# Performance work log

Hardware: AMD Instinct MI355X
Metric: run time of the kernel (lower is better)

The kernel has to match this reference:

```python
import jax, jax.numpy as jnp
import numpy as np


def _hadamard(n: int) -> np.ndarray:
    # Sylvester construction; n must be a power of 2 (asserted in the torch source).
    H = np.array([[1.0]], dtype=np.float32)
    while H.shape[0] < n:
        H = np.block([[H, H], [H, -H]])
    return (H * (n ** -0.5)).astype(np.float32)


def _rotate_activation(x):
    # hadamard_transform(x, scale=D**-0.5) over the last dim; bf16 in/out like the CUDA kernel.
    D = x.shape[-1]
    H = jnp.asarray(_hadamard(D))
    return (x.astype(jnp.float32) @ H).astype(x.dtype)


def _cu_seqlen_kv_bounds(seq_lens, num_ctx_tokens):
    # Vectorized equivalent of compute_cu_seqlen_kv_bounds_nocache (repeat_interleave -> searchsorted).
    offsets = jnp.concatenate([jnp.zeros(1, jnp.int32), jnp.cumsum(seq_lens).astype(jnp.int32)])
    pos = jnp.arange(num_ctx_tokens, dtype=jnp.int32)
    batch_ids = jnp.searchsorted(offsets, pos, side='right').astype(jnp.int32) - 1
    ks = offsets[batch_ids]                 # start of this token's sequence in packed KV
    ke = ks + (pos - ks) + 1                # causal: local_position + 1 past the start
    return ks, ke


def setup_inputs() -> dict:
    key = jax.random.key(0)
    k1, k2, k3 = jax.random.split(key, 3)
    T, H, D = 2048, 16, 128
    q = jax.random.normal(k1, (T, H, D), dtype=jnp.bfloat16)
    k = jax.random.normal(k2, (T, D), dtype=jnp.bfloat16)
    weights = jax.random.uniform(k3, (T, H), dtype=jnp.float32) * (H ** -0.5)
    seq_lens = jnp.array([1024, 1024], dtype=jnp.int32)
    return {"q": q, "k": k, "weights": weights, "seq_lens": seq_lens, "index_topk": 256}


def reference(q, k, weights, seq_lens, index_topk):
    T = q.shape[0]
    # Hadamard-rotate q and k (lightning indexer activation rotation).
    qr = _rotate_activation(q).astype(jnp.float32)   # [T, H, D]
    kr = _rotate_activation(k).astype(jnp.float32)   # [T, D]
    # Index score: I[t, s] = sum_h w[t, h] * relu(q[t, h] . k[s])
    logits = jnp.einsum('thd,sd->ths', qr, kr)       # [T, H, T]
    scores = jnp.einsum('ths,th->ts', jax.nn.relu(logits), weights)  # [T, T]
    # Causal ragged-batch KV window per token.
    ks, ke = _cu_seqlen_kv_bounds(seq_lens, T)
    pos = jnp.arange(T, dtype=jnp.int32)
    valid = (pos[None, :] >= ks[:, None]) & (pos[None, :] < ke[:, None])
    NEG = jnp.float32(-1e30)
    masked = jnp.where(valid, scores, NEG)
    topk_vals, topk_idx = jax.lax.top_k(masked, index_topk)  # [T, topk]
    return topk_vals, topk_idx
```

## Files before the change

kernel.cpp:

```cpp
#include <hip/hip_runtime.h>
#include <hip/hip_bf16.h>
#include <stdint.h>

typedef __attribute__((ext_vector_type(8))) short short8;
typedef __attribute__((ext_vector_type(4))) float float4_t;

#define DDIM 128
#define SORTN 256
#define LROW 136
#define SCAP 1088
#define NCHT 17

__device__ inline unsigned short f32_to_bf16_rne(float f) {
    uint32_t u = __float_as_uint(f);
    return (unsigned short)((u + 0x7FFFu + ((u >> 16) & 1u)) >> 16);
}
__device__ inline float bf16_to_f32(unsigned short h) {
    return __uint_as_float(((uint32_t)h) << 16);
}
__device__ inline int ks_of(const int* seq_lens, int n_seq, int t) {
    int off = 0, r = 0;
    for (int i = 0; i < n_seq; ++i) {
        int nx = off + seq_lens[i];
        if (t < nx) { r = off; break; }
        off = nx;
    }
    return r;
}

__device__ inline int wave_reduce_add_dpp(int x) {
    x += __builtin_amdgcn_update_dpp(0, x, 0x111, 0xF, 0xF, true);
    x += __builtin_amdgcn_update_dpp(0, x, 0x112, 0xF, 0xF, true);
    x += __builtin_amdgcn_update_dpp(0, x, 0x114, 0xF, 0xF, true);
    x += __builtin_amdgcn_update_dpp(0, x, 0x118, 0xF, 0xF, true);
    x += __builtin_amdgcn_update_dpp(0, x, 0x142, 0xA, 0xF, true);
    x += __builtin_amdgcn_update_dpp(0, x, 0x143, 0xC, 0xF, true);
    return __builtin_amdgcn_readlane(x, 63);
}

__global__ __launch_bounds__(256) void rotate_k_kernel(
        const unsigned short* __restrict__ k, unsigned short* __restrict__ kr, int T) {
    int row = blockIdx.x * 16 + (threadIdx.x >> 4);
    if (row >= T) return;
    int l16 = threadIdx.x & 15;
    short8 in = *(const short8*)(k + (size_t)row * DDIM + 8 * l16);
    float f[8];
    #pragma unroll
    for (int j = 0; j < 8; ++j) f[j] = bf16_to_f32((unsigned short)in[j]);
    #pragma unroll
    for (int b = 1; b <= 4; b <<= 1)
        #pragma unroll
        for (int j = 0; j < 8; ++j)
            if (!(j & b)) { float a = f[j], c = f[j | b]; f[j] = a + c; f[j | b] = a - c; }
    #pragma unroll
    for (int m = 1; m <= 8; m <<= 1) {
        bool hi = (l16 & m) != 0;
        #pragma unroll
        for (int j = 0; j < 8; ++j) {
            float o = __shfl_xor(f[j], m, 64);
            f[j] = hi ? (o - f[j]) : (f[j] + o);
        }
    }
    const float sc = 0.08838834764831845f;
    short8 out;
    #pragma unroll
    for (int j = 0; j < 8; ++j) out[j] = (short)f32_to_bf16_rne(f[j] * sc);
    *(short8*)(kr + (size_t)row * DDIM + 8 * l16) = out;
}

__global__ __launch_bounds__(512, 4) void fused_kernel(
        const unsigned short* __restrict__ q,
        const unsigned short* __restrict__ kr,
        const float* __restrict__ w,
        const int* __restrict__ seq_lens, int n_seq,
        float* __restrict__ out_vals, float* __restrict__ out_idx,
        int T, int H, int K, int Tt) {
    __shared__ __align__(16) unsigned short bL[2][64 * LROW];
    __shared__ __align__(16) float scw[4][SCAP];

    const int tid  = threadIdx.x;
    const int wv   = tid >> 6, lane = tid & 63;
    const int tok  = wv & 3, half = wv >> 2;
    const int col  = lane & 15, kgrp = lane >> 4;
    const int srow = tid >> 4, sseg = tid & 15;

    const int m     = blockIdx.x;
    const int ttile = (m & 1) ? (Tt - 1 - (m >> 1)) : (m >> 1);
    const int tt0   = ttile * 4;
    const int t_w   = tt0 + tok;
    const bool wvalid = (t_w < T);
    const int t_c  = wvalid ? t_w : T - 1;
    const int ks_w = ks_of(seq_lens, n_seq, t_c);
    const int ke_w = t_c + 1;
    const int n    = ke_w - ks_w;

    const int bks    = ks_of(seq_lens, n_seq, tt0);
    const int bke    = (tt0 + 4 < T) ? (tt0 + 4) : T;
    const int nchunk = (bke - bks + 63) >> 6;

    short8 pre[2];
    #pragma unroll
    for (int it = 0; it < 2; ++it) {
        int gs = bks + srow + 32 * it; if (gs > T - 1) gs = T - 1;
        pre[it] = *(const short8*)(kr + (size_t)gs * DDIM + sseg * 8);
    }

    float f[4][8];
    const unsigned short* qrow = q + ((size_t)t_c * H + col) * DDIM + kgrp * 8;
    #pragma unroll
    for (int kk = 0; kk < 4; ++kk) {
        short8 v = *(const short8*)(qrow + kk * 32);
        #pragma unroll
        for (int j = 0; j < 8; ++j) f[kk][j] = bf16_to_f32((unsigned short)v[j]);
    }
    #pragma unroll
    for (int b = 1; b <= 4; b <<= 1)
        #pragma unroll
        for (int kk = 0; kk < 4; ++kk)
            #pragma unroll
            for (int j = 0; j < 8; ++j)
                if (!(j & b)) { float a = f[kk][j], c = f[kk][j | b];
                                f[kk][j] = a + c; f[kk][j | b] = a - c; }
    #pragma unroll
    for (int kk = 0; kk < 4; ++kk)
        #pragma unroll
        for (int j = 0; j < 8; ++j) {
            float o = __shfl_xor(f[kk][j], 16, 64);
            f[kk][j] = (kgrp & 1) ? (o - f[kk][j]) : (f[kk][j] + o);
        }
    #pragma unroll
    for (int kk = 0; kk < 4; ++kk)
        #pragma unroll
        for (int j = 0; j < 8; ++j) {
            float o = __shfl_xor(f[kk][j], 32, 64);
            f[kk][j] = (kgrp & 2) ? (o - f[kk][j]) : (f[kk][j] + o);
        }
    #pragma unroll
    for (int j = 0; j < 8; ++j) {
        { float a = f[0][j], c = f[1][j]; f[0][j] = a + c; f[1][j] = a - c; }
        { float a = f[2][j], c = f[3][j]; f[2][j] = a + c; f[3][j] = a - c; }
        { float a = f[0][j], c = f[2][j]; f[0][j] = a + c; f[2][j] = a - c; }
        { float a = f[1][j], c = f[3][j]; f[1][j] = a + c; f[3][j] = a - c; }
    }
    short8 afrag[4];
    const float scl = 0.08838834764831845f;
    #pragma unroll
    for (int kk = 0; kk < 4; ++kk)
        #pragma unroll
        for (int j = 0; j < 8; ++j)
            afrag[kk][j] = (short)f32_to_bf16_rne(f[kk][j] * scl);

    float w4[4];
    #pragma unroll
    for (int r = 0; r < 4; ++r) w4[r] = w[(size_t)t_c * H + kgrp * 4 + r];

    #pragma unroll
    for (int it = 0; it < 2; ++it)
        *(short8*)&bL[0][(srow + 32 * it) * LROW + sseg * 8] = pre[it];
    __syncthreads();

    for (int c = 0; c < nchunk; ++c) {
        const int kv0 = bks + c * 64;
        if (c + 1 < nchunk) {
            int kvn = kv0 + 64;
            #pragma unroll
            for (int it = 0; it < 2; ++it) {
                int gs = kvn + srow + 32 * it; if (gs > T - 1) gs = T - 1;
                pre[it] = *(const short8*)(kr + (size_t)gs * DDIM + sseg * 8);
            }
        }
        const unsigned short* sb = bL[c & 1];
        #pragma unroll
        for (int nth = 0; nth < 2; ++nth) {
            const int nt = half * 2 + nth;
            float4_t acc = {0.f, 0.f, 0.f, 0.f};
            #pragma unroll
            for (int kk = 0; kk < 4; ++kk) {
                short8 bf = *(const short8*)&sb[(nt * 16 + col) * LROW + kgrp * 8 + kk * 32];
                acc = __builtin_amdgcn_mfma_f32_16x16x32_bf16(afrag[kk], bf, acc, 0, 0, 0);
            }
            float p = 0.f;
            #pragma unroll
            for (int r = 0; r < 4; ++r) {
                float v = acc[r];
                v = v > 0.f ? v : 0.f;
                p += w4[r] * v;
            }
            p += __shfl_xor(p, 16, 64);
            p += __shfl_xor(p, 32, 64);
            int s = kv0 + nt * 16 + col;
            if (wvalid && lane < 16 && s >= ks_w && s <= t_w)
                scw[tok][s - ks_w] = p;
        }
        if (c + 1 < nchunk) {
            #pragma unroll
            for (int it = 0; it < 2; ++it)
                *(short8*)&bL[(c + 1) & 1][(srow + 32 * it) * LROW + sseg * 8] = pre[it];
        }
        __syncthreads();
    }

    if (half == 1 || !wvalid) return;

    const int nch = (n + 63) >> 6;
    uint32_t ukey[NCHT];
    #pragma unroll
    for (int c = 0; c < NCHT; ++c) {
        if (c < nch) {
            int i = c * 64 + lane;
            ukey[c] = (i < n) ? __float_as_uint(scw[tok][i]) : 0u;
        } else ukey[c] = 0u;
    }
    unsigned long long* candw = (unsigned long long*)&scw[tok][0];

    const int Keff = (n < K) ? n : K;
    uint32_t ustar = 0;
    int ttake = K;
    if (n > K) {
        uint32_t lo = 0, hi = 0x80000000u;
        for (int it = 0; it < 31; ++it) {
            uint32_t mid = (lo + hi) >> 1;
            int lc = 0;
            #pragma unroll
            for (int c = 0; c < NCHT; ++c)
                if (c < nch) lc += (ukey[c] >= mid) ? 1 : 0;
            int total = wave_reduce_add_dpp(lc);
            if (total >= K) lo = mid; else hi = mid;
        }
        ustar = lo;
        int lg = 0;
        #pragma unroll
        for (int c = 0; c < NCHT; ++c)
            if (c < nch) lg += (ukey[c] > ustar) ? 1 : 0;
        ttake = K - wave_reduce_add_dpp(lg);
    }

    {
        const unsigned long long ltm = (1ull << lane) - 1ull;
        int base = 0, tieBase = 0;
        const bool selAll = (n <= K);
        #pragma unroll
        for (int c = 0; c < NCHT; ++c) {
            if (c < nch) {
                int i = c * 64 + lane;
                bool inb = (i < n);
                uint32_t u = ukey[c];
                bool isGt  = inb && (selAll || u > ustar);
                bool isTie = inb && !selAll && (u == ustar);
                unsigned long long mt = __ballot(isTie);
                int tr = tieBase + (int)__popcll(mt & ltm);
                bool take = isGt || (isTie && tr < ttake);
                unsigned long long mk = __ballot(take);
                if (take) {
                    int pos = base + (int)__popcll(mk & ltm);
                    int s = ks_w + i;
                    if (pos < SORTN)
                        candw[pos] = ((((unsigned long long)u << 11) |
                                       (unsigned long long)(T - 1 - s)) + 1ull);
                }
                base    += (int)__popcll(mk);
                tieBase += (int)__popcll(mt);
            }
        }
        for (int i = Keff + lane; i < SORTN; i += 64) candw[i] = 0ull;
    }

    unsigned long long kreg[4];
    #pragma unroll
    for (int r = 0; r < 4; ++r) kreg[r] = candw[4 * lane + r];

    #define CX(a, b, dsc) { unsigned long long _mx = (a) > (b) ? (a) : (b); \
                            unsigned long long _mn = (a) > (b) ? (b) : (a); \
                            (a) = (dsc) ? _mx : _mn; (b) = (dsc) ? _mn : _mx; }
    #pragma unroll
    for (int size = 2; size <= SORTN; size <<= 1) {
        #pragma unroll
        for (int stride = SORTN >> 1; stride >= 4; stride >>= 1) {
            if (stride > (size >> 1)) continue;
            int lmask = stride >> 2;
            #pragma unroll
            for (int r = 0; r < 4; ++r) {
                int e = 4 * lane + r;
                unsigned long long other = __shfl_xor(kreg[r], lmask, 64);
                bool desc = ((e & size) == 0);
                bool iAmLow = ((e & stride) == 0);
                bool keepMax = (iAmLow == desc);
                kreg[r] = keepMax ? (kreg[r] > other ? kreg[r] : other)
                                  : (kreg[r] < other ? kreg[r] : other);
            }
        }
        if (size >= 4) {
            bool d = (((4 * lane) & size) == 0);
            CX(kreg[0], kreg[2], d);
            CX(kreg[1], kreg[3], d);
            CX(kreg[0], kreg[1], d);
            CX(kreg[2], kreg[3], d);
        } else {
            CX(kreg[0], kreg[1], true);
            CX(kreg[2], kreg[3], false);
        }
    }
    #undef CX

    if (4 * lane < K) {
        float4_t v4, i4;
        #pragma unroll
        for (int r = 0; r < 4; ++r) {
            int e = 4 * lane + r;
            unsigned long long key = kreg[r];
            float v; int idx;
            if (key != 0ull) {
                unsigned long long km1 = key - 1ull;
                v = __uint_as_float((uint32_t)(km1 >> 11));
                idx = T - 1 - (int)(km1 & 0x7FFull);
            } else {
                int pidx = e - Keff;
                idx = (pidx < ks_w) ? pidx : (ke_w + (pidx - ks_w));
                v = -1e30f;
            }
            v4[r] = v; i4[r] = (float)idx;
        }
        *(float4_t*)(out_vals + (size_t)t_w * K + 4 * lane) = v4;
        *(float4_t*)(out_idx  + (size_t)t_w * K + 4 * lane) = i4;
    }
}

extern "C" void kernel_launch(void* const* d_in, const int* in_sizes, int n_in,
                              void* d_out, int out_size, void* d_ws, size_t ws_size,
                              hipStream_t stream) {
    const unsigned short* q = (const unsigned short*)d_in[0];
    const unsigned short* k = (const unsigned short*)d_in[1];
    const float* w          = (const float*)d_in[2];
    const int* seq_lens     = (const int*)d_in[3];
    const int n_seq = in_sizes[3];
    const int T = in_sizes[1] / DDIM;
    const int H = in_sizes[2] / T;
    const int K = out_size / (2 * T);

    unsigned short* kr = (unsigned short*)d_ws;
    float* out_vals = (float*)d_out;
    float* out_idx  = out_vals + (size_t)T * K;

    rotate_k_kernel<<<dim3((T + 15) / 16), dim3(256), 0, stream>>>(k, kr, T);
    const int Tt = (T + 3) / 4;
    fused_kernel<<<dim3(Tt), dim3(512), 0, stream>>>(
        q, kr, w, seq_lens, n_seq, out_vals, out_idx, T, H, K, Tt);
}
```

Measured before the change: 104.1 us.

## Switch score GEMM to 32x32x16 MFMA with two tokens per wave

The block shrinks from 512 to 256 threads (4 waves). Rotated q is staged through shared memory so each wave holds A fragments for two tokens (32 head rows) and computes a 32-row KV tile with 32x32x16 bf16 MFMAs instead of 16x16x32 ones. Weighted ReLU reduction now needs a single cross-lane shuffle per token, and the MFMA loop is wrapped in s_setprio. Each wave then runs top-k for one token, so all waves do useful selection work, at the cost of more registers per lane and an extra barrier.

```diff
diff --git a/kernel.cpp b/kernel.cpp
--- a/kernel.cpp
+++ b/kernel.cpp
@@ -4,6 +4,7 @@
 
 typedef __attribute__((ext_vector_type(8))) short short8;
 typedef __attribute__((ext_vector_type(4))) float float4_t;
+typedef __attribute__((ext_vector_type(16))) float float16_t;
 
 #define DDIM 128
 #define SORTN 256
@@ -68,7 +69,7 @@
     *(short8*)(kr + (size_t)row * DDIM + 8 * l16) = out;
 }
 
-__global__ __launch_bounds__(512, 4) void fused_kernel(
+__global__ __launch_bounds__(256, 2) void fused_kernel(
         const unsigned short* __restrict__ q,
         const unsigned short* __restrict__ kr,
         const float* __restrict__ w,
@@ -77,36 +78,39 @@
         int T, int H, int K, int Tt) {
     __shared__ __align__(16) unsigned short bL[2][64 * LROW];
     __shared__ __align__(16) float scw[4][SCAP];
+    unsigned short* qst = (unsigned short*)&scw[0][0];
 
     const int tid  = threadIdx.x;
     const int wv   = tid >> 6, lane = tid & 63;
-    const int tok  = wv & 3, half = wv >> 2;
+    const int pair = wv & 1, rowtile = wv >> 1;
     const int col  = lane & 15, kgrp = lane >> 4;
+    const int hi   = lane >> 5;
     const int srow = tid >> 4, sseg = tid & 15;
 
     const int m     = blockIdx.x;
     const int ttile = (m & 1) ? (Tt - 1 - (m >> 1)) : (m >> 1);
     const int tt0   = ttile * 4;
-    const int t_w   = tt0 + tok;
-    const bool wvalid = (t_w < T);
-    const int t_c  = wvalid ? t_w : T - 1;
-    const int ks_w = ks_of(seq_lens, n_seq, t_c);
-    const int ke_w = t_c + 1;
-    const int n    = ke_w - ks_w;
+
+    const int tAg = tt0 + pair * 2, tBg = tAg + 1;
+    const bool vA = (tAg < T), vB = (tBg < T);
+    const int tA  = vA ? tAg : T - 1, tB = vB ? tBg : T - 1;
+    const int ksA = ks_of(seq_lens, n_seq, tA);
+    const int ksB = ks_of(seq_lens, n_seq, tB);
 
     const int bks    = ks_of(seq_lens, n_seq, tt0);
     const int bke    = (tt0 + 4 < T) ? (tt0 + 4) : T;
     const int nchunk = (bke - bks + 63) >> 6;
 
-    short8 pre[2];
-    #pragma unroll
-    for (int it = 0; it < 2; ++it) {
-        int gs = bks + srow + 32 * it; if (gs > T - 1) gs = T - 1;
+    short8 pre[4];
+    #pragma unroll
+    for (int it = 0; it < 4; ++it) {
+        int gs = bks + srow + 16 * it; if (gs > T - 1) gs = T - 1;
         pre[it] = *(const short8*)(kr + (size_t)gs * DDIM + sseg * 8);
     }
 
+    const int t_r = (tt0 + wv < T) ? (tt0 + wv) : (T - 1);
     float f[4][8];
-    const unsigned short* qrow = q + ((size_t)t_c * H + col) * DDIM + kgrp * 8;
+    const unsigned short* qrow = q + ((size_t)t_r * H + col) * DDIM + kgrp * 8;
     #pragma unroll
     for (int kk = 0; kk < 4; ++kk) {
         short8 v = *(const short8*)(qrow + kk * 32);
@@ -142,65 +146,83 @@
         { float a = f[0][j], c = f[2][j]; f[0][j] = a + c; f[2][j] = a - c; }
         { float a = f[1][j], c = f[3][j]; f[1][j] = a + c; f[3][j] = a - c; }
     }
-    short8 afrag[4];
     const float scl = 0.08838834764831845f;
     #pragma unroll
-    for (int kk = 0; kk < 4; ++kk)
-        #pragma unroll
-        for (int j = 0; j < 8; ++j)
-            afrag[kk][j] = (short)f32_to_bf16_rne(f[kk][j] * scl);
-
-    float w4[4];
-    #pragma unroll
-    for (int r = 0; r < 4; ++r) w4[r] = w[(size_t)t_c * H + kgrp * 4 + r];
-
-    #pragma unroll
-    for (int it = 0; it < 2; ++it)
-        *(short8*)&bL[0][(srow + 32 * it) * LROW + sseg * 8] = pre[it];
+    for (int kk = 0; kk < 4; ++kk) {
+        short8 o;
+        #pragma unroll
+        for (int j = 0; j < 8; ++j) o[j] = (short)f32_to_bf16_rne(f[kk][j] * scl);
+        *(short8*)&qst[(wv * 16 + col) * LROW + kgrp * 8 + kk * 32] = o;
+    }
+
+    #pragma unroll
+    for (int it = 0; it < 4; ++it)
+        *(short8*)&bL[0][(srow + 16 * it) * LROW + sseg * 8] = pre[it];
     __syncthreads();
 
+    short8 afrag[8];
+    {
+        const unsigned short* qr2 = qst + (pair * 32 + (lane & 31)) * LROW + hi * 8;
+        #pragma unroll
+        for (int k8 = 0; k8 < 8; ++k8) afrag[k8] = *(const short8*)(qr2 + 16 * k8);
+    }
+    float wAr[8], wBr[8];
+    #pragma unroll
+    for (int r = 0; r < 8; ++r) {
+        int h = (r & 3) + 8 * ((r >> 2) & 1) + 4 * hi;
+        wAr[r] = w[(size_t)tA * H + h];
+        wBr[r] = w[(size_t)tB * H + h];
+    }
+    __syncthreads();
+
+    const int nrow = rowtile * 32 + (lane & 31);
     for (int c = 0; c < nchunk; ++c) {
         const int kv0 = bks + c * 64;
         if (c + 1 < nchunk) {
             int kvn = kv0 + 64;
             #pragma unroll
-            for (int it = 0; it < 2; ++it) {
-                int gs = kvn + srow + 32 * it; if (gs > T - 1) gs = T - 1;
+            for (int it = 0; it < 4; ++it) {
+                int gs = kvn + srow + 16 * it; if (gs > T - 1) gs = T - 1;
                 pre[it] = *(const short8*)(kr + (size_t)gs * DDIM + sseg * 8);
             }
         }
-        const unsigned short* sb = bL[c & 1];
-        #pragma unroll
-        for (int nth = 0; nth < 2; ++nth) {
-            const int nt = half * 2 + nth;
-            float4_t acc = {0.f, 0.f, 0.f, 0.f};
-            #pragma unroll
-            for (int kk = 0; kk < 4; ++kk) {
-                short8 bf = *(const short8*)&sb[(nt * 16 + col) * LROW + kgrp * 8 + kk * 32];
-                acc = __builtin_amdgcn_mfma_f32_16x16x32_bf16(afrag[kk], bf, acc, 0, 0, 0);
-            }
-            float p = 0.f;
-            #pragma unroll
-            for (int r = 0; r < 4; ++r) {
-                float v = acc[r];
-                v = v > 0.f ? v : 0.f;
-                p += w4[r] * v;
-            }
-            p += __shfl_xor(p, 16, 64);
-            p += __shfl_xor(p, 32, 64);
-            int s = kv0 + nt * 16 + col;
-            if (wvalid && lane < 16 && s >= ks_w && s <= t_w)
-                scw[tok][s - ks_w] = p;
+        const unsigned short* brow = &bL[c & 1][nrow * LROW + hi * 8];
+        float16_t acc = {0.f, 0.f, 0.f, 0.f, 0.f, 0.f, 0.f, 0.f,
+                         0.f, 0.f, 0.f, 0.f, 0.f, 0.f, 0.f, 0.f};
+        __builtin_amdgcn_s_setprio(1);
+        #pragma unroll
+        for (int k8 = 0; k8 < 8; ++k8) {
+            short8 bf = *(const short8*)(brow + 16 * k8);
+            acc = __builtin_amdgcn_mfma_f32_32x32x16_bf16(afrag[k8], bf, acc, 0, 0, 0);
+        }
+        __builtin_amdgcn_s_setprio(0);
+        float pA = 0.f, pB = 0.f;
+        #pragma unroll
+        for (int r = 0; r < 8; ++r) {
+            float va = acc[r];     va = va > 0.f ? va : 0.f; pA += wAr[r] * va;
+            float vb = acc[r + 8]; vb = vb > 0.f ? vb : 0.f; pB += wBr[r] * vb;
+        }
+        pA += __shfl_xor(pA, 32, 64);
+        pB += __shfl_xor(pB, 32, 64);
+        const int s = kv0 + nrow;
+        if (hi == 0) {
+            if (vA && s >= ksA && s <= tA) scw[pair * 2][s - ksA] = pA;
+        } else {
+            if (vB && s >= ksB && s <= tB) scw[pair * 2 + 1][s - ksB] = pB;
         }
         if (c + 1 < nchunk) {
             #pragma unroll
-            for (int it = 0; it < 2; ++it)
-                *(short8*)&bL[(c + 1) & 1][(srow + 32 * it) * LROW + sseg * 8] = pre[it];
+            for (int it = 0; it < 4; ++it)
+                *(short8*)&bL[(c + 1) & 1][(srow + 16 * it) * LROW + sseg * 8] = pre[it];
         }
         __syncthreads();
     }
 
-    if (half == 1 || !wvalid) return;
+    const int t_s = tt0 + wv;
+    if (t_s >= T) return;
+    const int ks_w = ks_of(seq_lens, n_seq, t_s);
+    const int ke_w = t_s + 1;
+    const int n    = ke_w - ks_w;
 
     const int nch = (n + 63) >> 6;
     uint32_t ukey[NCHT];
@@ -208,24 +230,24 @@
     for (int c = 0; c < NCHT; ++c) {
         if (c < nch) {
             int i = c * 64 + lane;
-            ukey[c] = (i < n) ? __float_as_uint(scw[tok][i]) : 0u;
+            ukey[c] = (i < n) ? __float_as_uint(scw[wv][i]) : 0u;
         } else ukey[c] = 0u;
     }
-    unsigned long long* candw = (unsigned long long*)&scw[tok][0];
+    unsigned long long* candw = (unsigned long long*)&scw[wv][0];
 
     const int Keff = (n < K) ? n : K;
     uint32_t ustar = 0;
     int ttake = K;
     if (n > K) {
-        uint32_t lo = 0, hi = 0x80000000u;
+        uint32_t lo = 0, hia = 0x80000000u;
         for (int it = 0; it < 31; ++it) {
-            uint32_t mid = (lo + hi) >> 1;
+            uint32_t mid = (lo + hia) >> 1;
             int lc = 0;
             #pragma unroll
             for (int c = 0; c < NCHT; ++c)
                 if (c < nch) lc += (ukey[c] >= mid) ? 1 : 0;
             int total = wave_reduce_add_dpp(lc);
-            if (total >= K) lo = mid; else hi = mid;
+            if (total >= K) lo = mid; else hia = mid;
         }
         ustar = lo;
         int lg = 0;
@@ -320,8 +342,8 @@
             }
             v4[r] = v; i4[r] = (float)idx;
         }
-        *(float4_t*)(out_vals + (size_t)t_w * K + 4 * lane) = v4;
-        *(float4_t*)(out_idx  + (size_t)t_w * K + 4 * lane) = i4;
+        *(float4_t*)(out_vals + (size_t)t_s * K + 4 * lane) = v4;
+        *(float4_t*)(out_idx  + (size_t)t_s * K + 4 * lane) = i4;
     }
 }
 
@@ -343,6 +365,6 @@
 
     rotate_k_kernel<<<dim3((T + 15) / 16), dim3(256), 0, stream>>>(k, kr, T);
     const int Tt = (T + 3) / 4;
-    fused_kernel<<<dim3(Tt), dim3(512), 0, stream>>>(
+    fused_kernel<<<dim3(Tt), dim3(256), 0, stream>>>(
         q, kr, w, seq_lens, n_seq, out_vals, out_idx, T, H, K, Tt);
 }
```

Measured after the change: 101.2 us. 1.03x faster.
